# Optimization experiments

Hardware: AMD Instinct MI355X
Metric: run time of the kernel (lower is better)

The kernel has to match this reference:

```python
import jax, jax.numpy as jnp
import numpy as np

D_MODEL = 1024
D_STATE = 16
D_CONV = 4
EXPAND = 2
D_INNER = EXPAND * D_MODEL
DT_RANK = D_MODEL // 16  # ceil(1024/16) = 64
BSZ = 2
SEQ = 1024


def _silu(x):
    return x * jax.nn.sigmoid(x)


def _mamba(x, in_proj, conv_w, conv_b, x_proj, dt_w, dt_b, A_log, Dp, out_proj):
    """Single-direction Mamba block. x: (B, L, d_model)."""
    Bb, Ll, _ = x.shape
    xz = jnp.einsum('bld,ed->ble', x, in_proj)          # (B,L,2*d_inner)
    xi, z = jnp.split(xz, 2, axis=-1)                   # (B,L,d_inner)
    # depthwise causal conv1d over L (kernel d_conv)
    xp = jnp.pad(xi, ((0, 0), (D_CONV - 1, 0), (0, 0)))
    xc = conv_b + sum(conv_w[:, k] * xp[:, k:k + Ll, :] for k in range(D_CONV))
    xc = _silu(xc)                                      # (B,L,d_inner)
    dbl = jnp.einsum('ble,fe->blf', xc, x_proj)         # (B,L,dt_rank+2*d_state)
    dt, Bm, Cm = jnp.split(dbl, [DT_RANK, DT_RANK + D_STATE], axis=-1)
    delta = jax.nn.softplus(jnp.einsum('blr,er->ble', dt, dt_w) + dt_b)  # (B,L,d_inner)
    A = -jnp.exp(A_log)                                 # (d_inner,d_state)
    dA = jnp.exp(delta[..., None] * A)                  # (B,L,E,N)
    dBu = (delta * xc)[..., None] * Bm[:, :, None, :]   # (B,L,E,N)
    def step(h, t):
        dA_t, dBu_t, C_t = t
        h = dA_t * h + dBu_t                            # (B,E,N)
        return h, jnp.einsum('ben,bn->be', h, C_t)
    h0 = jnp.zeros((Bb, D_INNER, D_STATE), x.dtype)
    _, ys = jax.lax.scan(step, h0, (dA.transpose(1, 0, 2, 3),
                                    dBu.transpose(1, 0, 2, 3),
                                    Cm.transpose(1, 0, 2)))
    y = ys.transpose(1, 0, 2) + xc * Dp                 # skip connection
    y = y * _silu(z)                                    # gate
    return jnp.einsum('ble,de->bld', y, out_proj)


def setup_inputs() -> dict:
    key = jax.random.key(0)
    ks = jax.random.split(key, 4)
    def nrm(k, shape, s=0.02):
        return s * jax.random.normal(k, shape, dtype=jnp.float32)
    def mamba_params(kb):
        k = jax.random.split(kb, 6)
        return dict(
            in_proj=nrm(k[0], (2 * D_INNER, D_MODEL)),
            conv_w=nrm(k[1], (D_INNER, D_CONV), 0.2),
            conv_b=jnp.zeros((D_INNER,), jnp.float32),
            x_proj=nrm(k[2], (DT_RANK + 2 * D_STATE, D_INNER)),
            dt_w=nrm(k[3], (D_INNER, DT_RANK), 0.1),
            dt_b=nrm(k[4], (D_INNER,), 0.5) - 4.0,  # softplus -> dt ~ 0.018
            A_log=jnp.log(jnp.broadcast_to(jnp.arange(1, D_STATE + 1, dtype=jnp.float32), (D_INNER, D_STATE))),
            D=jnp.ones((D_INNER,), jnp.float32),
            out_proj=nrm(k[5], (D_MODEL, D_INNER)),
        )
    inp = {'x': jax.random.normal(ks[2], (BSZ, SEQ, D_MODEL), dtype=jnp.float32)}
    for name, p in (('fwd', mamba_params(ks[0])), ('bwd', mamba_params(ks[1]))):
        for kk, v in p.items():
            inp[f'{name}_{kk}'] = v
    inp['merge_w'] = nrm(ks[3], (D_MODEL, 2 * D_MODEL))
    return inp


def reference(x,
              fwd_in_proj, fwd_conv_w, fwd_conv_b, fwd_x_proj, fwd_dt_w, fwd_dt_b,
              fwd_A_log, fwd_D, fwd_out_proj,
              bwd_in_proj, bwd_conv_w, bwd_conv_b, bwd_x_proj, bwd_dt_w, bwd_dt_b,
              bwd_A_log, bwd_D, bwd_out_proj,
              merge_w):
    f = _mamba(x, fwd_in_proj, fwd_conv_w, fwd_conv_b, fwd_x_proj, fwd_dt_w,
               fwd_dt_b, fwd_A_log, fwd_D, fwd_out_proj)
    b = _mamba(jnp.flip(x, 1), bwd_in_proj, bwd_conv_w, bwd_conv_b, bwd_x_proj,
               bwd_dt_w, bwd_dt_b, bwd_A_log, bwd_D, bwd_out_proj)
    b = jnp.flip(b, 1)
    return jnp.einsum('blf,df->bld', jnp.concatenate([f, b], axis=-1), merge_w)
```

## Files before the change

### kernel.cpp

```cpp
#include <hip/hip_runtime.h>
#include <math.h>

#define BSZ 2
#define SEQ 1024
#define DM  1024
#define DI  2048
#define DS  16
#define DC  4
#define DR  64
#define NDBL 96
#define NC  32
#define LC  32
#define MM  (BSZ * SEQ)

typedef unsigned short u16;
typedef __bf16 bf16x8 __attribute__((ext_vector_type(8)));
typedef float  f32x4  __attribute__((ext_vector_type(4)));

constexpr int N4_X   = MM * DM / 4;
constexpr int N4_MW  = DM * 2 * DM / 4;
constexpr int N4_IN  = 2 * DI * DM / 4;
constexpr int N4_XP  = NDBL * DI / 4;
constexpr int N4_DT  = DI * DR / 4;
constexpr int N4_OUT = DM * DI / 4;
constexpr int N4_TOTAL = N4_X + N4_MW + 2 * (N4_IN + N4_XP + N4_DT + N4_OUT);
constexpr size_t O_XP  = (size_t)2 * DI * DM;
constexpr size_t O_DT  = O_XP + (size_t)NDBL * DI;
constexpr size_t O_OUT = O_DT + (size_t)DI * DR;
constexpr size_t WBF_SZ = O_OUT + (size_t)DM * DI;

__device__ __forceinline__ u16 f2b(float f) {
    unsigned int u = __float_as_uint(f);
    unsigned int r = (u + 0x7fffu + ((u >> 16) & 1u)) >> 16;
    return (u16)r;
}
__device__ __forceinline__ float b2f(u16 h) {
    return __uint_as_float(((unsigned int)h) << 16);
}

__device__ __forceinline__ void stf(float* p, size_t i, float v) { p[i] = v; }
__device__ __forceinline__ void stf(u16* p, size_t i, float v)   { p[i] = f2b(v); }

__device__ __forceinline__ float fexp(float x)  { return __expf(x); }
__device__ __forceinline__ float frcp(float x)  { return __builtin_amdgcn_rcpf(x); }
__device__ __forceinline__ float silu_fast(float x) {
    return x * frcp(1.f + fexp(-x));
}
__device__ __forceinline__ float softplus_fast(float x) {
    return (x > 15.f) ? x : __logf(1.f + fexp(x));
}

__device__ __forceinline__ void async16(const u16* g, u16* l) {
    __builtin_amdgcn_global_load_lds(
        (const __attribute__((address_space(1))) void*)g,
        (__attribute__((address_space(3))) void*)l, 16, 0, 0);
}

__device__ __forceinline__ int lds_slot(int row, int j) {
    return row * 4 + ((j + (row >> 1)) & 3);
}

__device__ __forceinline__ void stage8f(const float* p, u16* d) {
    float4 v0 = *(const float4*)p;
    float4 v1 = *(const float4*)(p + 4);
    ushort4 a; a.x = f2b(v0.x); a.y = f2b(v0.y); a.z = f2b(v0.z); a.w = f2b(v0.w);
    ushort4 b; b.x = f2b(v1.x); b.y = f2b(v1.y); b.z = f2b(v1.z); b.w = f2b(v1.w);
    *(ushort4*)d = a;
    *(ushort4*)(d + 4) = b;
}

__global__ __launch_bounds__(256) void cvt_all_kernel(
    const float* __restrict__ s0, const float* __restrict__ s1,
    const float* __restrict__ s2, const float* __restrict__ s3,
    const float* __restrict__ s4, const float* __restrict__ s5,
    const float* __restrict__ s6, const float* __restrict__ s7,
    const float* __restrict__ s8, const float* __restrict__ s9,
    u16* __restrict__ d0, u16* __restrict__ d1, u16* __restrict__ d2,
    u16* __restrict__ d3, u16* __restrict__ d4, u16* __restrict__ d5,
    u16* __restrict__ d6, u16* __restrict__ d7, u16* __restrict__ d8,
    u16* __restrict__ d9)
{
    int i = blockIdx.x * 256 + threadIdx.x;
    const float* s; u16* d;
    if (i < N4_X) { s = s0; d = d0; }
    else if ((i -= N4_X) < N4_MW) { s = s1; d = d1; }
    else if ((i -= N4_MW) < N4_IN) { s = s2; d = d2; }
    else if ((i -= N4_IN) < N4_XP) { s = s3; d = d3; }
    else if ((i -= N4_XP) < N4_DT) { s = s4; d = d4; }
    else if ((i -= N4_DT) < N4_OUT) { s = s5; d = d5; }
    else if ((i -= N4_OUT) < N4_IN) { s = s6; d = d6; }
    else if ((i -= N4_IN) < N4_XP) { s = s7; d = d7; }
    else if ((i -= N4_XP) < N4_DT) { s = s8; d = d8; }
    else if ((i -= N4_DT) < N4_OUT) { s = s9; d = d9; }
    else return;
    float4 v = ((const float4*)s)[i];
    ushort4 o; o.x = f2b(v.x); o.y = f2b(v.y); o.z = f2b(v.z); o.w = f2b(v.w);
    ((ushort4*)d)[i] = o;
}

__global__ __launch_bounds__(512) void gemm256_dual(
    const u16* __restrict__ A,
    const u16* __restrict__ Wd0, const u16* __restrict__ Wd1,
    float* __restrict__ Cd0, float* __restrict__ Cd1,
    int lda, int ldw, int ldc, int K)
{
    __shared__ u16 lds[65536];
    const int t    = threadIdx.x;
    const int lane = t & 63;
    const int w    = t >> 6;
    const int wr   = w >> 2;
    const int wc   = w & 3;
    const int fm   = lane & 15;
    const int q    = lane >> 4;
    const int dir  = blockIdx.z;
    const u16* W   = dir ? Wd1 : Wd0;
    float* C       = dir ? Cd1 : Cd0;
    const int m0   = blockIdx.y * 256;
    const int n0   = blockIdx.x * 256;
    const int T    = K >> 6;

    int offA[4][2], offW[2][2];
    #pragma unroll
    for (int mi = 0; mi < 4; mi++)
        #pragma unroll
        for (int kk = 0; kk < 2; kk++) {
            int r = wr * 64 + mi * 16 + fm;
            int j = kk * 4 + q;
            offA[mi][kk] = (r * 8 + ((j + r) & 7)) * 8;
        }
    #pragma unroll
    for (int ni = 0; ni < 2; ni++)
        #pragma unroll
        for (int kk = 0; kk < 2; kk++) {
            int r = wc * 32 + ni * 16 + fm;
            int j = kk * 4 + q;
            offW[ni][kk] = (r * 8 + ((j + r) & 7)) * 8;
        }

    int sr[2], sj[2];
    #pragma unroll
    for (int p = 0; p < 2; p++) {
        int slot = p * 512 + t;
        sr[p] = slot >> 3;
        sj[p] = ((slot & 7) - sr[p]) & 7;
    }
    const int ldsWaveBase = (t & ~63) * 8;

#define STAGE(G, ld, row0, kcol, dstBase)                                    \
    { _Pragma("unroll")                                                      \
      for (int p = 0; p < 2; p++) {                                          \
          const u16* src_ = (G) + (size_t)((row0) + sr[p]) * (ld)            \
                          + (kcol) + sj[p] * 8;                              \
          async16(src_, &lds[(dstBase) + p * 4096 + ldsWaveBase]);           \
      } }

    f32x4 acc[2][2][4][2] = {};
    bf16x8 af[4][2], wf[2][2];

#define DSREAD_A(mh, cur)                                                    \
    { _Pragma("unroll")                                                      \
      for (int mi = 0; mi < 4; mi++)                                         \
          _Pragma("unroll")                                                  \
          for (int kk = 0; kk < 2; kk++)                                     \
              af[mi][kk] = *(const bf16x8*)&lds[(cur) + (mh) * 8192          \
                                                + offA[mi][kk]]; }
#define DSREAD_W(nh, cur)                                                    \
    { _Pragma("unroll")                                                      \
      for (int ni = 0; ni < 2; ni++)                                         \
          _Pragma("unroll")                                                  \
          for (int kk = 0; kk < 2; kk++)                                     \
              wf[ni][kk] = *(const bf16x8*)&lds[(cur) + 16384 + (nh) * 8192  \
                                                + offW[ni][kk]]; }
#define MFMA16(mh, nh)                                                       \
    { __builtin_amdgcn_s_setprio(1);                                         \
      _Pragma("unroll")                                                      \
      for (int mi = 0; mi < 4; mi++)                                         \
          _Pragma("unroll")                                                  \
          for (int ni = 0; ni < 2; ni++)                                     \
              _Pragma("unroll")                                              \
              for (int kk = 0; kk < 2; kk++)                                 \
                  acc[mh][nh][mi][ni] =                                      \
                      __builtin_amdgcn_mfma_f32_16x16x32_bf16(               \
                          af[mi][kk], wf[ni][kk], acc[mh][nh][mi][ni],       \
                          0, 0, 0);                                          \
      __builtin_amdgcn_s_setprio(0); }

#define WAITVM(n) asm volatile("s_waitcnt vmcnt(" #n ")" ::: "memory")
#define BAR() __builtin_amdgcn_s_barrier()

    STAGE(A, lda, m0,       0, 0);
    STAGE(W, ldw, n0,       0, 16384);
    STAGE(W, ldw, n0 + 128, 0, 16384 + 8192);
    STAGE(A, lda, m0 + 128, 0, 8192);
    WAITVM(4);
    BAR();

    for (int tt = 0; tt < T - 1; ++tt) {
        const int cur = (tt & 1) * 32768;
        const int nxt = 32768 - cur;
        const int kn  = (tt + 1) << 6;
        DSREAD_A(0, cur); DSREAD_W(0, cur);
        STAGE(A, lda, m0, kn, nxt);
        WAITVM(4);
        BAR();
        MFMA16(0, 0);
        BAR();
        DSREAD_W(1, cur);
        STAGE(W, ldw, n0, kn, nxt + 16384);
        WAITVM(4);
        BAR();
        MFMA16(0, 1);
        BAR();
        DSREAD_A(1, cur);
        STAGE(W, ldw, n0 + 128, kn, nxt + 16384 + 8192);
        BAR();
        MFMA16(1, 1);
        BAR();
        DSREAD_W(0, cur);
        STAGE(A, lda, m0 + 128, kn, nxt + 8192);
        WAITVM(4);
        BAR();
        MFMA16(1, 0);
        BAR();
    }
    {
        const int cur = ((T - 1) & 1) * 32768;
        DSREAD_A(0, cur); DSREAD_W(0, cur);
        WAITVM(2);
        BAR();
        MFMA16(0, 0);
        BAR();
        DSREAD_W(1, cur);
        WAITVM(0);
        BAR();
        MFMA16(0, 1);
        BAR();
        DSREAD_A(1, cur);
        BAR();
        MFMA16(1, 1);
        BAR();
        DSREAD_W(0, cur);
        MFMA16(1, 0);
    }
#undef STAGE
#undef DSREAD_A
#undef DSREAD_W
#undef MFMA16
#undef WAITVM
#undef BAR

    #pragma unroll
    for (int mh = 0; mh < 2; mh++)
        #pragma unroll
        for (int mi = 0; mi < 4; mi++)
            #pragma unroll
            for (int rr = 0; rr < 4; rr++) {
                int gm = m0 + mh * 128 + wr * 64 + mi * 16 + q * 4 + rr;
                int om = gm;
                if (dir == 1) {
                    om = (gm & ~(SEQ - 1)) | ((SEQ - 1) - (gm & (SEQ - 1)));
                }
                float* crow = C + (size_t)om * ldc;
                #pragma unroll
                for (int nh = 0; nh < 2; nh++)
                    #pragma unroll
                    for (int ni = 0; ni < 2; ni++) {
                        int gn = n0 + nh * 128 + wc * 32 + ni * 16 + fm;
                        crow[gn] = acc[mh][nh][mi][ni][rr];
                    }
            }
}

template <typename TA, typename TC, int ACT, bool DUAL, bool FLIP1, int NSPLIT, int BN>
__global__ __launch_bounds__(256) void mfma_gemm(
    const TA* __restrict__ A0, const TA* __restrict__ A1, int lda,
    const u16* __restrict__ W0, const u16* __restrict__ W1, int ldw,
    const float* __restrict__ bias0, const float* __restrict__ bias1,
    TC* __restrict__ C0, TC* __restrict__ C1, int ldc,
    int M, int N, int K)
{
    constexpr int NF = BN / 32;
    __shared__ u16 As[128 * 32];
    __shared__ u16 Ws[BN * 32];

    const int z = blockIdx.z;
    const int dir = DUAL ? (z / NSPLIT) : 0;
    const int split = z % NSPLIT;
    const TA* A = dir ? A1 : A0;
    const u16* W = dir ? W1 : W0;
    const float* bias = dir ? bias1 : bias0;
    TC* C = dir ? C1 : C0;
    if (NSPLIT > 1) C += (size_t)split * M * ldc;
    const int kseg = K / NSPLIT;
    const int kbeg = split * kseg, kend = kbeg + kseg;

    const int t = threadIdx.x;
    const int wave = t >> 6;
    const int lane = t & 63;
    const int wm = (wave & 1) * 64;
    const int wn = (wave >> 1) * (BN / 2);
    const int fm = lane & 15;
    const int q  = lane >> 4;
    const int m0 = blockIdx.y * 128;
    const int n0 = blockIdx.x * BN;

    f32x4 acc[4][NF] = {};

    for (int k0 = kbeg; k0 < kend; k0 += 32) {
        if constexpr (__is_same(TA, u16)) {
            #pragma unroll
            for (int p = 0; p < 2; p++) {
                int i = p * 256 + wave * 64 + lane;
                int r = i >> 2;
                int j = ((i & 3) - (r >> 1)) & 3;
                async16(A + (size_t)(m0 + r) * lda + k0 + j * 8,
                        &As[(size_t)(p * 256 + wave * 64) * 8]);
            }
        } else {
            #pragma unroll
            for (int p = 0; p < 2; p++) {
                int i = p * 256 + t;
                int r = i >> 2;
                int j = ((i & 3) - (r >> 1)) & 3;
                stage8f(A + (size_t)(m0 + r) * lda + k0 + j * 8, &As[(size_t)i * 8]);
            }
        }
        #pragma unroll
        for (int p = 0; p < BN / 64; p++) {
            int i = p * 256 + wave * 64 + lane;
            int r = i >> 2;
            int j = ((i & 3) - (r >> 1)) & 3;
            int gr = n0 + r;
            if (gr >= N) gr = N - 1;
            async16(W + (size_t)gr * ldw + k0 + j * 8,
                    &Ws[(size_t)(p * 256 + wave * 64) * 8]);
        }
        __syncthreads();

        bf16x8 af[4], wf[NF];
        #pragma unroll
        for (int mi = 0; mi < 4; mi++)
            af[mi] = *(const bf16x8*)&As[(size_t)lds_slot(wm + mi * 16 + fm, q) * 8];
        #pragma unroll
        for (int ni = 0; ni < NF; ni++)
            wf[ni] = *(const bf16x8*)&Ws[(size_t)lds_slot(wn + ni * 16 + fm, q) * 8];
        #pragma unroll
        for (int mi = 0; mi < 4; mi++)
            #pragma unroll
            for (int ni = 0; ni < NF; ni++)
                acc[mi][ni] = __builtin_amdgcn_mfma_f32_16x16x32_bf16(
                    af[mi], wf[ni], acc[mi][ni], 0, 0, 0);
        __syncthreads();
    }

    const int rb = q * 4;
    const int cc = fm;
    #pragma unroll
    for (int mi = 0; mi < 4; mi++) {
        #pragma unroll
        for (int r = 0; r < 4; r++) {
            int gm = m0 + wm + mi * 16 + rb + r;
            int om = gm;
            if (FLIP1 && dir == 1) {
                int bb = gm / SEQ, l = gm % SEQ;
                om = bb * SEQ + (SEQ - 1 - l);
            }
            #pragma unroll
            for (int ni = 0; ni < NF; ni++) {
                int gn = n0 + wn + ni * 16 + cc;
                if (gn < N) {
                    float v = acc[mi][ni][r];
                    if (ACT == 1) v = softplus_fast(v + bias[gn]);
                    stf(C, (size_t)om * ldc + gn, v);
                }
            }
        }
    }
}

__global__ __launch_bounds__(256) void combine_dbl_kernel(
    const float* __restrict__ par, float* __restrict__ dbl)
{
    int i4 = blockIdx.x * 256 + threadIdx.x;
    const int per = (MM * NDBL) / 4;
    int dir = (i4 >= per) ? 1 : 0;
    int j4 = i4 - dir * per;
    const float* p = par + (size_t)dir * 4 * MM * NDBL;
    f32x4 s = {0.f, 0.f, 0.f, 0.f};
    #pragma unroll
    for (int k = 0; k < 4; k++)
        s += *(const f32x4*)&p[(size_t)k * MM * NDBL + (size_t)j4 * 4];
    *(f32x4*)&dbl[(size_t)dir * MM * NDBL + (size_t)j4 * 4] = s;
}

__global__ __launch_bounds__(256) void combine_cat_kernel(
    const float* __restrict__ par, u16* __restrict__ cat)
{
    int i4 = blockIdx.x * 256 + threadIdx.x;
    const int per = (MM * DM) / 4;
    int dir = (i4 >= per) ? 1 : 0;
    int j4 = i4 - dir * per;
    const float* p0 = par + (size_t)dir * 2 * MM * DM;
    const float* p1 = p0 + (size_t)MM * DM;
    f32x4 a = *(const f32x4*)&p0[(size_t)j4 * 4];
    f32x4 b = *(const f32x4*)&p1[(size_t)j4 * 4];
    int m = j4 >> 8;
    int n4 = j4 & 255;
    ushort4 o;
    o.x = f2b(a[0] + b[0]); o.y = f2b(a[1] + b[1]);
    o.z = f2b(a[2] + b[2]); o.w = f2b(a[3] + b[3]);
    *(ushort4*)&cat[(size_t)m * 2 * DM + dir * DM + n4 * 4] = o;
}

__global__ __launch_bounds__(256) void combine_out_kernel(
    const float* __restrict__ p0, float* __restrict__ out)
{
    int i4 = blockIdx.x * 256 + threadIdx.x;
    const float* p1 = p0 + (size_t)MM * DM;
    f32x4 a = *(const f32x4*)&p0[(size_t)i4 * 4];
    f32x4 b = *(const f32x4*)&p1[(size_t)i4 * 4];
    *(f32x4*)&out[(size_t)i4 * 4] = a + b;
}

__global__ __launch_bounds__(256) void conv_silu_kernel(
    const float* __restrict__ xz,
    const float* __restrict__ cw0, const float* __restrict__ cw1,
    const float* __restrict__ cb0, const float* __restrict__ cb1,
    u16* __restrict__ xcb)
{
    int i4 = blockIdx.x * 256 + threadIdx.x;
    const int per = MM * DI / 4;
    int dir = (i4 >= per) ? 1 : 0;
    int rem = i4 - dir * per;
    int e4 = rem & (DI / 4 - 1);
    int bl = rem / (DI / 4);
    int l = bl & (SEQ - 1);
    int e = e4 * 4;
    const float* xz_d = xz + (size_t)dir * MM * 2 * DI;
    const float* cw = dir ? cw1 : cw0;
    const float* cb = dir ? cb1 : cb0;
    f32x4 cwv[4];
    #pragma unroll
    for (int i = 0; i < 4; i++) cwv[i] = *(const f32x4*)&cw[(e + i) * DC];
    f32x4 acc = *(const f32x4*)&cb[e];
    #pragma unroll
    for (int k = 0; k < DC; k++) {
        int ll = l + k - (DC - 1);
        if (ll >= 0) {
            f32x4 xv = *(const f32x4*)&xz_d[(size_t)(bl - l + ll) * (2 * DI) + e];
            #pragma unroll
            for (int i = 0; i < 4; i++) acc[i] += cwv[i][k] * xv[i];
        }
    }
    ushort4 o;
    #pragma unroll
    for (int i = 0; i < 4; i++) {
        float s = silu_fast(acc[i]);
        ((u16*)&o)[i] = f2b(s);
    }
    ((ushort4*)xcb)[(size_t)dir * per + rem] = o;
}

__global__ __launch_bounds__(256) void scan_pass1(
    const float* __restrict__ dbl,
    const u16*  __restrict__ xc,
    const u16*  __restrict__ delta,
    const float* __restrict__ Alog0, const float* __restrict__ Alog1,
    float* __restrict__ Pout, float* __restrict__ Qout)
{
    __shared__ float sB[LC][16];
    const int t = threadIdx.x;
    const int c = blockIdx.x;
    const int dir = blockIdx.z >> 1;
    const int b = blockIdx.z & 1;
    const int e = blockIdx.y * 256 + t;
    const int row0 = b * SEQ + c * LC;
    const float* dbl_d = dbl + (size_t)dir * MM * NDBL;
    const u16* xc_d = xc + (size_t)dir * MM * DI;
    const u16* delta_d = delta + (size_t)dir * MM * DI;
    const float* A_log = dir ? Alog1 : Alog0;
    float* P_d = Pout + (size_t)dir * BSZ * NC * DI * DS;
    float* Q_d = Qout + (size_t)dir * BSZ * NC * DI * DS;

    if (t < LC * 4) {
        int row = t >> 2, col = (t & 3) * 4;
        *(f32x4*)&sB[row][col] =
            *(const f32x4*)&dbl_d[(size_t)(row0 + row) * NDBL + DR + col];
    }

    f32x4 Aen[4], P[4], Q[4];
    #pragma unroll
    for (int g = 0; g < 4; g++) {
        f32x4 a = *(const f32x4*)&A_log[(size_t)e * DS + g * 4];
        #pragma unroll
        for (int j = 0; j < 4; j++) Aen[g][j] = -fexp(a[j]);
        P[g] = f32x4{1.f, 1.f, 1.f, 1.f};
        Q[g] = f32x4{0.f, 0.f, 0.f, 0.f};
    }
    __syncthreads();

    float dv = b2f(delta_d[(size_t)row0 * DI + e]);
    float xv = b2f(xc_d[(size_t)row0 * DI + e]);
    for (int i = 0; i < LC; i++) {
        int ip = (i + 1 < LC) ? (i + 1) : (LC - 1);
        float dvn = b2f(delta_d[(size_t)(row0 + ip) * DI + e]);
        float xvn = b2f(xc_d[(size_t)(row0 + ip) * DI + e]);
        float du = dv * xv;
        #pragma unroll
        for (int g = 0; g < 4; g++) {
            f32x4 Bv = *(const f32x4*)&sB[i][g * 4];
            #pragma unroll
            for (int j = 0; j < 4; j++) {
                float dA = fexp(dv * Aen[g][j]);
                P[g][j] *= dA;
                Q[g][j] = dA * Q[g][j] + du * Bv[j];
            }
        }
        dv = dvn; xv = xvn;
    }
    size_t base = ((size_t)(b * NC + c) * DI + e) * DS;
    #pragma unroll
    for (int g = 0; g < 4; g++) {
        *(f32x4*)&P_d[base + g * 4] = P[g];
        *(f32x4*)&Q_d[base + g * 4] = Q[g];
    }
}

__global__ __launch_bounds__(256) void scan_pass2(
    const float* __restrict__ P, const float* __restrict__ Q,
    float* __restrict__ H0)
{
    const int gid = blockIdx.x * 256 + threadIdx.x;
    const int dir = gid >> 16;
    const int loc = gid & 65535;
    const int b = loc >> 15;
    const int en = loc & (DI * DS - 1);
    size_t doff = (size_t)dir * BSZ * NC * DI * DS;
    float h = 0.f;
    for (int c = 0; c < NC; c++) {
        size_t idx = doff + ((size_t)(b * NC + c) * DI * DS) + en;
        H0[idx] = h;
        h = P[idx] * h + Q[idx];
    }
}

__global__ __launch_bounds__(256) void scan_pass3(
    const float* __restrict__ dbl,
    const u16*  __restrict__ xc,
    const float* __restrict__ xz,
    u16* delta_y,
    const float* __restrict__ Alog0, const float* __restrict__ Alog1,
    const float* __restrict__ Dp0, const float* __restrict__ Dp1,
    const float* __restrict__ H0)
{
    __shared__ float sBC[LC][32];
    const int t = threadIdx.x;
    const int c = blockIdx.x;
    const int dir = blockIdx.z >> 1;
    const int b = blockIdx.z & 1;
    const int e = blockIdx.y * 256 + t;
    const int row0 = b * SEQ + c * LC;
    const float* dbl_d = dbl + (size_t)dir * MM * NDBL;
    const u16* xc_d = xc + (size_t)dir * MM * DI;
    const float* xz_d = xz + (size_t)dir * MM * 2 * DI;
    u16* dy_d = delta_y + (size_t)dir * MM * DI;
    const float* A_log = dir ? Alog1 : Alog0;
    const float* Dp = dir ? Dp1 : Dp0;
    const float* H0_d = H0 + (size_t)dir * BSZ * NC * DI * DS;

    {
        int row = t >> 3, col = (t & 7) * 4;
        *(f32x4*)&sBC[row][col] =
            *(const f32x4*)&dbl_d[(size_t)(row0 + row) * NDBL + DR + col];
    }

    f32x4 Aen[4], h[4];
    size_t base = ((size_t)(b * NC + c) * DI + e) * DS;
    #pragma unroll
    for (int g = 0; g < 4; g++) {
        f32x4 a = *(const f32x4*)&A_log[(size_t)e * DS + g * 4];
        #pragma unroll
        for (int j = 0; j < 4; j++) Aen[g][j] = -fexp(a[j]);
        h[g] = *(const f32x4*)&H0_d[base + g * 4];
    }
    const float Dv = Dp[e];
    __syncthreads();

    float dv = b2f(dy_d[(size_t)row0 * DI + e]);
    float xv = b2f(xc_d[(size_t)row0 * DI + e]);
    float zv = xz_d[(size_t)row0 * (2 * DI) + DI + e];
    for (int i = 0; i < LC; i++) {
        int ip = (i + 1 < LC) ? (i + 1) : (LC - 1);
        float dvn = b2f(dy_d[(size_t)(row0 + ip) * DI + e]);
        float xvn = b2f(xc_d[(size_t)(row0 + ip) * DI + e]);
        float zvn = xz_d[(size_t)(row0 + ip) * (2 * DI) + DI + e];
        float du = dv * xv;
        f32x4 pv = {0.f, 0.f, 0.f, 0.f};
        #pragma unroll
        for (int g = 0; g < 4; g++) {
            f32x4 Bv = *(const f32x4*)&sBC[i][g * 4];
            f32x4 Cv = *(const f32x4*)&sBC[i][16 + g * 4];
            #pragma unroll
            for (int j = 0; j < 4; j++) {
                float dA = fexp(dv * Aen[g][j]);
                h[g][j] = dA * h[g][j] + du * Bv[j];
                pv[j] += h[g][j] * Cv[j];
            }
        }
        float p = pv[0] + pv[1] + pv[2] + pv[3];
        float y = (p + xv * Dv) * silu_fast(zv);
        dy_d[(size_t)(row0 + i) * DI + e] = f2b(y);
        dv = dvn; xv = xvn; zv = zvn;
    }
}

extern "C" void kernel_launch(void* const* d_in, const int* in_sizes, int n_in,
                              void* d_out, int out_size, void* d_ws, size_t ws_size,
                              hipStream_t stream)
{
    const float* x = (const float*)d_in[0];
    const float* in_p[2]  = {(const float*)d_in[1],  (const float*)d_in[10]};
    const float* conv_w[2]= {(const float*)d_in[2],  (const float*)d_in[11]};
    const float* conv_b[2]= {(const float*)d_in[3],  (const float*)d_in[12]};
    const float* x_p[2]   = {(const float*)d_in[4],  (const float*)d_in[13]};
    const float* dt_w[2]  = {(const float*)d_in[5],  (const float*)d_in[14]};
    const float* dt_b[2]  = {(const float*)d_in[6],  (const float*)d_in[15]};
    const float* A_log[2] = {(const float*)d_in[7],  (const float*)d_in[16]};
    const float* Dp[2]    = {(const float*)d_in[8],  (const float*)d_in[17]};
    const float* out_p[2] = {(const float*)d_in[9],  (const float*)d_in[18]};
    const float* merge_w  = (const float*)d_in[19];
    float* out = (float*)d_out;

    float* ws = (float*)d_ws;
    float* ws_xz  = ws;
    float* ws_dbl = ws_xz  + (size_t)2 * MM * 2 * DI;
    float* ws_P   = ws_dbl + (size_t)2 * MM * NDBL;
    float* ws_Q   = ws_P   + (size_t)2 * BSZ * NC * DI * DS;
    float* ws_H0  = ws_Q   + (size_t)2 * BSZ * NC * DI * DS;
    u16* ws_delta = (u16*)(ws_H0 + (size_t)2 * BSZ * NC * DI * DS);
    u16* ws_xcb   = ws_delta + (size_t)2 * MM * DI;
    u16* ws_cat   = ws_xcb   + (size_t)2 * MM * DI;
    u16* ws_xbf   = ws_cat   + (size_t)MM * 2 * DM;
    u16* wbf_mw   = ws_xbf   + (size_t)MM * DM;
    u16* wbf0     = wbf_mw   + (size_t)DM * 2 * DM;
    u16* wbf1     = wbf0     + WBF_SZ;
    float* ws_par = ws_P;

    cvt_all_kernel<<<(N4_TOTAL + 255) / 256, 256, 0, stream>>>(
        x, merge_w, in_p[0], x_p[0], dt_w[0], out_p[0],
        in_p[1], x_p[1], dt_w[1], out_p[1],
        ws_xbf, wbf_mw,
        wbf0, wbf0 + O_XP, wbf0 + O_DT, wbf0 + O_OUT,
        wbf1, wbf1 + O_XP, wbf1 + O_DT, wbf1 + O_OUT);

    gemm256_dual<<<dim3(16, 8, 2), 512, 0, stream>>>(
        ws_xbf, wbf0, wbf1,
        ws_xz, ws_xz + (size_t)MM * 2 * DI,
        DM, DM, 2 * DI, DM);

    conv_silu_kernel<<<(2 * MM * DI / 4) / 256, 256, 0, stream>>>(
        ws_xz, conv_w[0], conv_w[1], conv_b[0], conv_b[1], ws_xcb);

    mfma_gemm<u16, float, 0, true, false, 4, 64><<<dim3(2, 16, 8), 256, 0, stream>>>(
        ws_xcb, ws_xcb + (size_t)MM * DI, DI,
        wbf0 + O_XP, wbf1 + O_XP, DI, nullptr, nullptr,
        ws_par, ws_par + (size_t)4 * MM * NDBL, NDBL, MM, NDBL, DI);
    combine_dbl_kernel<<<(2 * MM * NDBL / 4) / 256, 256, 0, stream>>>(ws_par, ws_dbl);

    mfma_gemm<float, u16, 1, true, false, 1, 64><<<dim3(32, 16, 2), 256, 0, stream>>>(
        ws_dbl, ws_dbl + (size_t)MM * NDBL, NDBL,
        wbf0 + O_DT, wbf1 + O_DT, DR, dt_b[0], dt_b[1],
        ws_delta, ws_delta + (size_t)MM * DI, DI, MM, DI, DR);

    {
        dim3 grid(NC, DI / 256, 2 * BSZ);
        scan_pass1<<<grid, 256, 0, stream>>>(ws_dbl, ws_xcb, ws_delta,
                                             A_log[0], A_log[1], ws_P, ws_Q);
        scan_pass2<<<(2 * BSZ * DI * DS) / 256, 256, 0, stream>>>(ws_P, ws_Q, ws_H0);
        scan_pass3<<<grid, 256, 0, stream>>>(ws_dbl, ws_xcb, ws_xz, ws_delta,
                                             A_log[0], A_log[1], Dp[0], Dp[1], ws_H0);
    }

    mfma_gemm<u16, float, 0, true, true, 2, 64><<<dim3(16, 16, 4), 256, 0, stream>>>(
        ws_delta, ws_delta + (size_t)MM * DI, DI,
        wbf0 + O_OUT, wbf1 + O_OUT, DI, nullptr, nullptr,
        ws_par, ws_par + (size_t)2 * MM * DM, DM, MM, DM, DI);
    combine_cat_kernel<<<(2 * MM * DM / 4) / 256, 256, 0, stream>>>(ws_par, ws_cat);

    mfma_gemm<u16, float, 0, false, false, 2, 64><<<dim3(16, 16, 2), 256, 0, stream>>>(
        ws_cat, ws_cat, 2 * DM, wbf_mw, wbf_mw, 2 * DM, nullptr, nullptr,
        ws_par, ws_par, DM, MM, DM, 2 * DM);
    combine_out_kernel<<<(MM * DM / 4) / 256, 256, 0, stream>>>(ws_par, out);
}
```

Before: 375.7 us.

## Store in_proj output as bf16 and write out_proj directly into concat buffer

The in_proj GEMM now writes its xz result as bf16 instead of fp32. The conv and scan kernels read it through bf16 loads, which halves the traffic for that large intermediate. The out_proj GEMM also drops its split-K into fp32 partials plus the combine kernel, and writes bf16 straight into the interleaved concat buffer with half as many blocks. The costs are lower precision on xz and z, and less parallelism in the out_proj GEMM because it no longer uses split-K.

New measurement: 367.8 us. -2.1%, faster.

```diff
diff --git a/kernel.cpp b/kernel.cpp
--- a/kernel.cpp
+++ b/kernel.cpp
@@ -101,7 +101,7 @@
 __global__ __launch_bounds__(512) void gemm256_dual(
     const u16* __restrict__ A,
     const u16* __restrict__ Wd0, const u16* __restrict__ Wd1,
-    float* __restrict__ Cd0, float* __restrict__ Cd1,
+    u16* __restrict__ Cd0, u16* __restrict__ Cd1,
     int lda, int ldw, int ldc, int K)
 {
     __shared__ u16 lds[65536];
@@ -114,7 +114,7 @@
     const int q    = lane >> 4;
     const int dir  = blockIdx.z;
     const u16* W   = dir ? Wd1 : Wd0;
-    float* C       = dir ? Cd1 : Cd0;
+    u16* C         = dir ? Cd1 : Cd0;
     const int m0   = blockIdx.y * 256;
     const int n0   = blockIdx.x * 256;
     const int T    = K >> 6;
@@ -260,13 +260,13 @@
                 if (dir == 1) {
                     om = (gm & ~(SEQ - 1)) | ((SEQ - 1) - (gm & (SEQ - 1)));
                 }
-                float* crow = C + (size_t)om * ldc;
+                u16* crow = C + (size_t)om * ldc;
                 #pragma unroll
                 for (int nh = 0; nh < 2; nh++)
                     #pragma unroll
                     for (int ni = 0; ni < 2; ni++) {
                         int gn = n0 + nh * 128 + wc * 32 + ni * 16 + fm;
-                        crow[gn] = acc[mh][nh][mi][ni][rr];
+                        crow[gn] = f2b(acc[mh][nh][mi][ni][rr]);
                     }
             }
 }
@@ -393,25 +393,6 @@
     *(f32x4*)&dbl[(size_t)dir * MM * NDBL + (size_t)j4 * 4] = s;
 }
 
-__global__ __launch_bounds__(256) void combine_cat_kernel(
-    const float* __restrict__ par, u16* __restrict__ cat)
-{
-    int i4 = blockIdx.x * 256 + threadIdx.x;
-    const int per = (MM * DM) / 4;
-    int dir = (i4 >= per) ? 1 : 0;
-    int j4 = i4 - dir * per;
-    const float* p0 = par + (size_t)dir * 2 * MM * DM;
-    const float* p1 = p0 + (size_t)MM * DM;
-    f32x4 a = *(const f32x4*)&p0[(size_t)j4 * 4];
-    f32x4 b = *(const f32x4*)&p1[(size_t)j4 * 4];
-    int m = j4 >> 8;
-    int n4 = j4 & 255;
-    ushort4 o;
-    o.x = f2b(a[0] + b[0]); o.y = f2b(a[1] + b[1]);
-    o.z = f2b(a[2] + b[2]); o.w = f2b(a[3] + b[3]);
-    *(ushort4*)&cat[(size_t)m * 2 * DM + dir * DM + n4 * 4] = o;
-}
-
 __global__ __launch_bounds__(256) void combine_out_kernel(
     const float* __restrict__ p0, float* __restrict__ out)
 {
@@ -423,7 +404,7 @@
 }
 
 __global__ __launch_bounds__(256) void conv_silu_kernel(
-    const float* __restrict__ xz,
+    const u16* __restrict__ xz,
     const float* __restrict__ cw0, const float* __restrict__ cw1,
     const float* __restrict__ cb0, const float* __restrict__ cb1,
     u16* __restrict__ xcb)
@@ -436,7 +417,7 @@
     int bl = rem / (DI / 4);
     int l = bl & (SEQ - 1);
     int e = e4 * 4;
-    const float* xz_d = xz + (size_t)dir * MM * 2 * DI;
+    const u16* xz_d = xz + (size_t)dir * MM * 2 * DI;
     const float* cw = dir ? cw1 : cw0;
     const float* cb = dir ? cb1 : cb0;
     f32x4 cwv[4];
@@ -447,9 +428,11 @@
     for (int k = 0; k < DC; k++) {
         int ll = l + k - (DC - 1);
         if (ll >= 0) {
-            f32x4 xv = *(const f32x4*)&xz_d[(size_t)(bl - l + ll) * (2 * DI) + e];
-            #pragma unroll
-            for (int i = 0; i < 4; i++) acc[i] += cwv[i][k] * xv[i];
+            ushort4 xv = *(const ushort4*)&xz_d[(size_t)(bl - l + ll) * (2 * DI) + e];
+            acc[0] += cwv[0][k] * b2f(xv.x);
+            acc[1] += cwv[1][k] * b2f(xv.y);
+            acc[2] += cwv[2][k] * b2f(xv.z);
+            acc[3] += cwv[3][k] * b2f(xv.w);
         }
     }
     ushort4 o;
@@ -547,7 +530,7 @@
 __global__ __launch_bounds__(256) void scan_pass3(
     const float* __restrict__ dbl,
     const u16*  __restrict__ xc,
-    const float* __restrict__ xz,
+    const u16*  __restrict__ xz,
     u16* delta_y,
     const float* __restrict__ Alog0, const float* __restrict__ Alog1,
     const float* __restrict__ Dp0, const float* __restrict__ Dp1,
@@ -562,7 +545,7 @@
     const int row0 = b * SEQ + c * LC;
     const float* dbl_d = dbl + (size_t)dir * MM * NDBL;
     const u16* xc_d = xc + (size_t)dir * MM * DI;
-    const float* xz_d = xz + (size_t)dir * MM * 2 * DI;
+    const u16* xz_d = xz + (size_t)dir * MM * 2 * DI;
     u16* dy_d = delta_y + (size_t)dir * MM * DI;
     const float* A_log = dir ? Alog1 : Alog0;
     const float* Dp = dir ? Dp1 : Dp0;
@@ -588,12 +571,12 @@
 
     float dv = b2f(dy_d[(size_t)row0 * DI + e]);
     float xv = b2f(xc_d[(size_t)row0 * DI + e]);
-    float zv = xz_d[(size_t)row0 * (2 * DI) + DI + e];
+    float zv = b2f(xz_d[(size_t)row0 * (2 * DI) + DI + e]);
     for (int i = 0; i < LC; i++) {
         int ip = (i + 1 < LC) ? (i + 1) : (LC - 1);
         float dvn = b2f(dy_d[(size_t)(row0 + ip) * DI + e]);
         float xvn = b2f(xc_d[(size_t)(row0 + ip) * DI + e]);
-        float zvn = xz_d[(size_t)(row0 + ip) * (2 * DI) + DI + e];
+        float zvn = b2f(xz_d[(size_t)(row0 + ip) * (2 * DI) + DI + e]);
         float du = dv * xv;
         f32x4 pv = {0.f, 0.f, 0.f, 0.f};
         #pragma unroll
@@ -632,12 +615,12 @@
     float* out = (float*)d_out;
 
     float* ws = (float*)d_ws;
-    float* ws_xz  = ws;
-    float* ws_dbl = ws_xz  + (size_t)2 * MM * 2 * DI;
+    float* ws_dbl = ws;
     float* ws_P   = ws_dbl + (size_t)2 * MM * NDBL;
     float* ws_Q   = ws_P   + (size_t)2 * BSZ * NC * DI * DS;
     float* ws_H0  = ws_Q   + (size_t)2 * BSZ * NC * DI * DS;
-    u16* ws_delta = (u16*)(ws_H0 + (size_t)2 * BSZ * NC * DI * DS);
+    u16* ws_xz    = (u16*)(ws_H0 + (size_t)2 * BSZ * NC * DI * DS);
+    u16* ws_delta = ws_xz    + (size_t)2 * MM * 2 * DI;
     u16* ws_xcb   = ws_delta + (size_t)2 * MM * DI;
     u16* ws_cat   = ws_xcb   + (size_t)2 * MM * DI;
     u16* ws_xbf   = ws_cat   + (size_t)MM * 2 * DM;
@@ -681,11 +664,10 @@
                                              A_log[0], A_log[1], Dp[0], Dp[1], ws_H0);
     }
 
-    mfma_gemm<u16, float, 0, true, true, 2, 64><<<dim3(16, 16, 4), 256, 0, stream>>>(
+    mfma_gemm<u16, u16, 0, true, true, 1, 64><<<dim3(16, 16, 2), 256, 0, stream>>>(
         ws_delta, ws_delta + (size_t)MM * DI, DI,
         wbf0 + O_OUT, wbf1 + O_OUT, DI, nullptr, nullptr,
-        ws_par, ws_par + (size_t)2 * MM * DM, DM, MM, DM, DI);
-    combine_cat_kernel<<<(2 * MM * DM / 4) / 256, 256, 0, stream>>>(ws_par, ws_cat);
+        ws_cat, ws_cat + DM, 2 * DM, MM, DM, DI);
 
     mfma_gemm<u16, float, 0, false, false, 2, 64><<<dim3(16, 16, 2), 256, 0, stream>>>(
         ws_cat, ws_cat, 2 * DM, wbf_mw, wbf_mw, 2 * DM, nullptr, nullptr,
```
